# Kernel optimization log

Measured on AMD Instinct MI355X. Metric: run time of the kernel, lower is better.

The kernel has to match this reference:

```python
import jax, jax.numpy as jnp
import numpy as np
from jax import lax

B, T1, T2, C = 8, 128, 128, 256
K = 3

def setup_inputs() -> dict:
    key = jax.random.key(0)
    k1, k2, kw, kb = jax.random.split(key, 4)
    x1 = jax.random.normal(k1, (B, T1, C), dtype=jnp.float32)
    x2 = jax.random.normal(k2, (B, T2, C), dtype=jnp.float32)
    # conv2d: in_channels = 2C, out_channels = C, kernel 3x3 (OIHW)
    fan_in = 2 * C * K * K
    bound = 1.0 / np.sqrt(fan_in)
    W = jax.random.uniform(kw, (C, 2 * C, K, K), jnp.float32, -bound, bound)
    b = jax.random.uniform(kb, (C,), jnp.float32, -bound, bound)
    alpha = jnp.float32(0.5)
    return {"x1": x1, "x2": x2, "W": W, "b": b, "alpha": alpha}


def reference(x1, x2, W, b, alpha):
    # x1: [B, T1, C], x2: [B, T2, C]
    a = jnp.transpose(x1, (0, 2, 1))  # [B, C, T1]
    c2 = jnp.transpose(x2, (0, 2, 1))  # [B, C, T2]
    Bd, Cd, T1d = a.shape
    T2d = c2.shape[-1]
    # joint outer-product tensor: [B, 2C, T1, T2]
    j1 = jnp.broadcast_to(a[:, :, :, None], (Bd, Cd, T1d, T2d))
    j2 = jnp.broadcast_to(c2[:, :, None, :], (Bd, Cd, T1d, T2d))
    joint = jnp.concatenate([j1, j2], axis=1)
    out = lax.conv_general_dilated(
        joint, W, window_strides=(1, 1), padding="SAME",
        dimension_numbers=("NCHW", "OIHW", "NCHW"))
    out = out + b[None, :, None, None]
    out = jax.nn.gelu(out, approximate=False)  # torch nn.GELU default = exact erf
    out_T1 = jnp.mean(out, axis=-1)            # [B, C, T1]
    out_T1 = jnp.transpose(out_T1, (0, 2, 1))  # [B, T1, C]
    return out_T1 * alpha + x1
```

## Files before the change

### kernel.cpp

```cpp
#include <hip/hip_runtime.h>
#include <math.h>

#define B_   8
#define T_   128
#define C_   256
#define XLDP 136

typedef unsigned short ushort;
typedef ushort ushort8v __attribute__((ext_vector_type(8)));
typedef __bf16 bf16x8  __attribute__((ext_vector_type(8)));
typedef float  f32x4   __attribute__((ext_vector_type(4)));

__device__ __forceinline__ ushort f2bf(float f) {
    unsigned u = __float_as_uint(f);
    u += 0x7fffu + ((u >> 16) & 1u);
    return (ushort)(u >> 16);
}

__device__ __forceinline__ float gelu_fast(float x) {
    float x2 = x * x;
    float y2 = x * fmaf(-0.10294234f, x2, -2.30220818f);
    float e  = __builtin_amdgcn_exp2f(y2);
    return x * __builtin_amdgcn_rcpf(1.0f + e);
}

__global__ __launch_bounds__(256) void tc_pack(
    const float* __restrict__ x1, const float* __restrict__ x2,
    const float* __restrict__ W, ushort* __restrict__ Xp,
    ushort* __restrict__ Wt)
{
    const int bid = blockIdx.x, t = threadIdx.x;
    if (bid < 256) {
        __shared__ ushort lw[4608];
        const float* src = W + (size_t)bid * 4608;
        #pragma unroll
        for (int i = 0; i < 18; ++i)
            lw[t + i * 256] = f2bf(src[t + i * 256]);
        __syncthreads();
        #pragma unroll
        for (int i = 0; i < 18; ++i) {
            int d = t + i * 256;
            int c = d & 255;
            int row18 = d >> 8;
            int s = (row18 >= 9) ? 1 : 0;
            int r = row18 - s * 9;
            int rsrc = (s == 0) ? r : (r % 3) * 3 + (r / 3);
            Wt[(((size_t)s * 64 + (bid >> 2)) * 48 + (bid & 3) * 9 + r) * 256 + c]
                = lw[(s * 256 + c) * 9 + rsrc];
        }
    } else {
        int g = (bid - 256) * 256 + t;
        int e = g * 8;
        int s  = e >> 18;
        int me = e & 262143;
        const float* src = (s ? x2 : x1) + me;
        float4 lo = *(const float4*)src;
        float4 hi = *(const float4*)(src + 4);
        ushort8v u;
        u[0] = f2bf(lo.x); u[1] = f2bf(lo.y); u[2] = f2bf(lo.z); u[3] = f2bf(lo.w);
        u[4] = f2bf(hi.x); u[5] = f2bf(hi.y); u[6] = f2bf(hi.z); u[7] = f2bf(hi.w);
        *(ushort8v*)&Xp[e] = u;
    }
}

__global__ __launch_bounds__(256, 4) void tc_gemm(
    const ushort* __restrict__ Xp, const ushort* __restrict__ Wt,
    float* __restrict__ Sg)
{
    __shared__ ushort Xs[64 * XLDP];
    __shared__ ushort Ws[48 * XLDP];

    const int og = blockIdx.x;
    const int mh = blockIdx.y;
    const int tid = threadIdx.x;
    const int l = tid & 63, w = tid >> 6;
    const int r16 = l & 15, kb = l >> 4;

    ushort8v xb[2][4], wb[2][3];
    f32x4 acc[2][3] = {};

    auto loadr = [&](int r, int buf) {
        int s = r >> 1, p = r & 1;
        const ushort* xsrc = Xp + ((size_t)s * 1024 + mh * 64) * 256 + p * 128;
        #pragma unroll
        for (int j = 0; j < 4; ++j) {
            int c = tid + j * 256;
            xb[buf][j] = *(const ushort8v*)(xsrc + (size_t)(c >> 4) * 256 + (c & 15) * 8);
        }
        const ushort* wsrc = Wt + ((size_t)s * 64 + og) * 48 * 256 + p * 128;
        #pragma unroll
        for (int j = 0; j < 3; ++j) {
            int c = tid + j * 256;
            wb[buf][j] = *(const ushort8v*)(wsrc + (size_t)(c >> 4) * 256 + (c & 15) * 8);
        }
    };

    loadr(0, 0);

    #pragma unroll
    for (int r = 0; r < 4; ++r) {
        const int cur = r & 1, s = r >> 1;
        __syncthreads();
        #pragma unroll
        for (int j = 0; j < 4; ++j) {
            int c = tid + j * 256;
            *(ushort8v*)&Xs[(c >> 4) * XLDP + (c & 15) * 8] = xb[cur][j];
        }
        #pragma unroll
        for (int j = 0; j < 3; ++j) {
            int c = tid + j * 256;
            *(ushort8v*)&Ws[(c >> 4) * XLDP + (c & 15) * 8] = wb[cur][j];
        }
        if (r < 3) loadr(r + 1, cur ^ 1);
        __syncthreads();
        #pragma unroll
        for (int ks = 0; ks < 4; ++ks) {
            bf16x8 af = __builtin_bit_cast(bf16x8,
                *(const ushort8v*)&Xs[(w * 16 + r16) * XLDP + ks * 32 + kb * 8]);
            #pragma unroll
            for (int nf = 0; nf < 3; ++nf) {
                bf16x8 bfr = __builtin_bit_cast(bf16x8,
                    *(const ushort8v*)&Ws[(nf * 16 + r16) * XLDP + ks * 32 + kb * 8]);
                acc[s][nf] = __builtin_amdgcn_mfma_f32_16x16x32_bf16(af, bfr, acc[s][nf], 0, 0, 0);
            }
        }
    }

    #pragma unroll
    for (int s = 0; s < 2; ++s)
        #pragma unroll
        for (int nf = 0; nf < 3; ++nf) {
            int n = nf * 16 + r16;
            if (n < 36)
                *(f32x4*)&Sg[((size_t)(s * 64 + og) * 36 + n) * 1024
                             + mh * 64 + w * 16 + kb * 4] = acc[s][nf];
        }
}

__global__ __launch_bounds__(128) void tc_fin(
    const float* __restrict__ Sg, const float* __restrict__ x1,
    const float* __restrict__ bias, const float* __restrict__ alpha_p,
    float* __restrict__ out)
{
    const int o = blockIdx.x & 255;
    const int b = blockIdx.x >> 8;
    const int t = threadIdx.x;
    const int og = o >> 2, oo = o & 3;

    __shared__ float Bv[3][T_];

    const float* S0 = Sg + ((size_t)og * 36 + oo * 9) * 1024 + b * 128;
    const float* S1 = Sg + ((size_t)(64 + og) * 36 + oo * 9) * 1024 + b * 128;

    float a0 = 0.f, a1 = 0.f, a2 = 0.f;
    float b0 = 0.f, b1 = 0.f, b2 = 0.f;
    #pragma unroll
    for (int sh = 0; sh < 3; ++sh) {
        int row = t + sh - 1;
        if (row >= 0 && row < T_) {
            const float* p0 = S0 + sh * 3 * 1024 + row;
            a0 += p0[0]; a1 += p0[1024]; a2 += p0[2048];
            const float* p1 = S1 + sh * 3 * 1024 + row;
            b0 += p1[0]; b1 += p1[1024]; b2 += p1[2048];
        }
    }
    const float bo = bias[o];
    float A3 = bo + a0 + a1 + a2;
    float Al = bo + a1 + a2;
    float Ar = bo + a0 + a1;
    Bv[0][t] = b0 + b1 + b2;
    Bv[1][t] = b1 + b2;
    Bv[2][t] = b0 + b1;
    __syncthreads();

    int cls = (t == 0) ? 1 : ((t == T_ - 1) ? 2 : 0);
    const float* Bs = Bv[cls];
    float s0 = 0.f, s1 = 0.f, s2 = 0.f, s3 = 0.f;
    for (int j = 0; j < T_; j += 4) {
        f32x4 v = *(const f32x4*)&Bs[j];
        s0 += gelu_fast(A3 + v[0]); s1 += gelu_fast(A3 + v[1]);
        s2 += gelu_fast(A3 + v[2]); s3 += gelu_fast(A3 + v[3]);
    }
    float sm = (s0 + s1) + (s2 + s3);
    float bl = Bs[0], br = Bs[T_ - 1];
    sm += gelu_fast(Al + bl) - gelu_fast(A3 + bl);
    sm += gelu_fast(Ar + br) - gelu_fast(A3 + br);

    const float kk2 = (*alpha_p) * (1.0f / (float)T_);
    size_t go = ((size_t)(b * T_ + t)) * C_ + o;
    out[go] = sm * kk2 + x1[go];
}

extern "C" void kernel_launch(void* const* d_in, const int* in_sizes, int n_in,
                              void* d_out, int out_size, void* d_ws, size_t ws_size,
                              hipStream_t stream) {
    const float* x1    = (const float*)d_in[0];
    const float* x2    = (const float*)d_in[1];
    const float* W     = (const float*)d_in[2];
    const float* bias  = (const float*)d_in[3];
    const float* alpha = (const float*)d_in[4];
    float* out = (float*)d_out;

    float*  Sg = (float*)d_ws;
    ushort* Xp = (ushort*)((char*)d_ws + (size_t)2 * 64 * 36 * 1024 * 4);
    ushort* Wt = Xp + (size_t)2 * 1024 * 256;

    tc_pack<<<512, 256, 0, stream>>>(x1, x2, W, Xp, Wt);
    tc_gemm<<<dim3(64, 16), 256, 0, stream>>>(Xp, Wt, Sg);
    tc_fin<<<B_ * C_, T_, 0, stream>>>(Sg, x1, bias, alpha, out);
}
```

Before: 94.81 us.

## Fold time-shift reduction into GEMM K dimension via halo-padded X tile

The GEMM is reorganized so the three time-shifted taps are summed inside the MFMA K loop. The kernel loads a 66-row X tile with zero-padded halo and indexes it with a shift offset, using K=768 instead of writing 36 separate partial products per output group. Weights are repacked accordingly, and the grid becomes 12x16x2 with 64x64 tiles and a 2x2 warp layout. The finisher now reads 3 precomputed values per side instead of gathering and summing 9 shifted values, which cuts intermediate traffic. The cost is a larger shared-memory footprint and lower occupancy (launch bounds 3).

```diff
diff --git a/kernel.cpp b/kernel.cpp
--- a/kernel.cpp
+++ b/kernel.cpp
@@ -4,7 +4,8 @@
 #define B_   8
 #define T_   128
 #define C_   256
-#define XLDP 136
+#define XLDS 264
+#define WLDP 136
 
 typedef unsigned short ushort;
 typedef ushort ushort8v __attribute__((ext_vector_type(8)));
@@ -39,14 +40,15 @@
         __syncthreads();
         #pragma unroll
         for (int i = 0; i < 18; ++i) {
-            int d = t + i * 256;
-            int c = d & 255;
-            int row18 = d >> 8;
-            int s = (row18 >= 9) ? 1 : 0;
-            int r = row18 - s * 9;
-            int rsrc = (s == 0) ? r : (r % 3) * 3 + (r / 3);
-            Wt[(((size_t)s * 64 + (bid >> 2)) * 48 + (bid & 3) * 9 + r) * 256 + c]
-                = lw[(s * 256 + c) * 9 + rsrc];
+            int d  = t + i * 256;
+            int s  = d / 2304;
+            int e  = d - s * 2304;
+            int nj = e / 768;
+            int k  = e - nj * 768;
+            int sh = k >> 8, ci = k & 255;
+            ushort v = (s == 0) ? lw[ci * 9 + sh * 3 + nj]
+                                : lw[(256 + ci) * 9 + nj * 3 + sh];
+            Wt[((size_t)s * 768 + bid * 3 + nj) * 768 + k] = v;
         }
     } else {
         int g = (bid - 256) * 256 + t;
@@ -63,107 +65,115 @@
     }
 }
 
-__global__ __launch_bounds__(256, 4) void tc_gemm(
+__global__ __launch_bounds__(256, 3) void tc_gemm(
     const ushort* __restrict__ Xp, const ushort* __restrict__ Wt,
-    float* __restrict__ Sg)
+    float* __restrict__ AB)
 {
-    __shared__ ushort Xs[64 * XLDP];
-    __shared__ ushort Ws[48 * XLDP];
-
-    const int og = blockIdx.x;
-    const int mh = blockIdx.y;
-    const int tid = threadIdx.x;
-    const int l = tid & 63, w = tid >> 6;
+    __shared__ ushort Xs[66 * XLDS];
+    __shared__ ushort Ws[64 * WLDP];
+
+    const int tn = blockIdx.x;
+    const int tm = blockIdx.y;
+    const int s  = blockIdx.z;
+    const int u  = threadIdx.x;
+    const int l  = u & 63, w = u >> 6;
+    const int wr = w >> 1, wc = w & 1;
     const int r16 = l & 15, kb = l >> 4;
 
-    ushort8v xb[2][4], wb[2][3];
-    f32x4 acc[2][3] = {};
-
-    auto loadr = [&](int r, int buf) {
-        int s = r >> 1, p = r & 1;
-        const ushort* xsrc = Xp + ((size_t)s * 1024 + mh * 64) * 256 + p * 128;
+    const int b_     = tm >> 1;
+    const int t_base = (tm & 1) * 64;
+    const ushort* Xb = Xp + ((size_t)s * 1024 + b_ * T_) * C_;
+    const ushort* Wb = Wt + ((size_t)s * 768 + tn * 64) * 768;
+
+    {
+        ushort8v zero = {};
+        #pragma unroll
+        for (int j = 0; j < 9; ++j) {
+            int c = u + j * 256;
+            if (j < 8 || c < 2112) {
+                int i  = c >> 5;
+                int kc = (c & 31) * 8;
+                int t  = t_base + i - 1;
+                ushort8v v = (t >= 0 && t < T_)
+                           ? *(const ushort8v*)(Xb + (size_t)t * C_ + kc) : zero;
+                *(ushort8v*)&Xs[i * XLDS + kc] = v;
+            }
+        }
+    }
+
+    ushort8v wbuf[4];
+    #pragma unroll
+    for (int j = 0; j < 4; ++j) {
+        int c = u + j * 256;
+        wbuf[j] = *(const ushort8v*)(Wb + (size_t)(c >> 4) * 768 + (c & 15) * 8);
+    }
+
+    f32x4 acc[2][2] = {};
+    #pragma unroll
+    for (int r = 0; r < 6; ++r) {
+        const int sh = r >> 1, p = r & 1;
+        __syncthreads();
         #pragma unroll
         for (int j = 0; j < 4; ++j) {
-            int c = tid + j * 256;
-            xb[buf][j] = *(const ushort8v*)(xsrc + (size_t)(c >> 4) * 256 + (c & 15) * 8);
-        }
-        const ushort* wsrc = Wt + ((size_t)s * 64 + og) * 48 * 256 + p * 128;
-        #pragma unroll
-        for (int j = 0; j < 3; ++j) {
-            int c = tid + j * 256;
-            wb[buf][j] = *(const ushort8v*)(wsrc + (size_t)(c >> 4) * 256 + (c & 15) * 8);
-        }
-    };
-
-    loadr(0, 0);
+            int c = u + j * 256;
+            *(ushort8v*)&Ws[(c >> 4) * WLDP + (c & 15) * 8] = wbuf[j];
+        }
+        if (r < 5) {
+            const int rn = r + 1;
+            const ushort* wsrc = Wb + (rn >> 1) * 256 + (rn & 1) * 128;
+            #pragma unroll
+            for (int j = 0; j < 4; ++j) {
+                int c = u + j * 256;
+                wbuf[j] = *(const ushort8v*)(wsrc + (size_t)(c >> 4) * 768 + (c & 15) * 8);
+            }
+        }
+        __syncthreads();
+        #pragma unroll
+        for (int ks = 0; ks < 4; ++ks) {
+            const int ka = p * 128 + ks * 32 + kb * 8;
+            const int kw_ = ks * 32 + kb * 8;
+            bf16x8 a0 = __builtin_bit_cast(bf16x8,
+                *(const ushort8v*)&Xs[(wr * 32 + r16 + sh) * XLDS + ka]);
+            bf16x8 a1 = __builtin_bit_cast(bf16x8,
+                *(const ushort8v*)&Xs[(wr * 32 + 16 + r16 + sh) * XLDS + ka]);
+            bf16x8 b0 = __builtin_bit_cast(bf16x8,
+                *(const ushort8v*)&Ws[(wc * 32 + r16) * WLDP + kw_]);
+            bf16x8 b1 = __builtin_bit_cast(bf16x8,
+                *(const ushort8v*)&Ws[(wc * 32 + 16 + r16) * WLDP + kw_]);
+            acc[0][0] = __builtin_amdgcn_mfma_f32_16x16x32_bf16(a0, b0, acc[0][0], 0, 0, 0);
+            acc[0][1] = __builtin_amdgcn_mfma_f32_16x16x32_bf16(a0, b1, acc[0][1], 0, 0, 0);
+            acc[1][0] = __builtin_amdgcn_mfma_f32_16x16x32_bf16(a1, b0, acc[1][0], 0, 0, 0);
+            acc[1][1] = __builtin_amdgcn_mfma_f32_16x16x32_bf16(a1, b1, acc[1][1], 0, 0, 0);
+        }
+    }
 
     #pragma unroll
-    for (int r = 0; r < 4; ++r) {
-        const int cur = r & 1, s = r >> 1;
-        __syncthreads();
-        #pragma unroll
-        for (int j = 0; j < 4; ++j) {
-            int c = tid + j * 256;
-            *(ushort8v*)&Xs[(c >> 4) * XLDP + (c & 15) * 8] = xb[cur][j];
-        }
-        #pragma unroll
-        for (int j = 0; j < 3; ++j) {
-            int c = tid + j * 256;
-            *(ushort8v*)&Ws[(c >> 4) * XLDP + (c & 15) * 8] = wb[cur][j];
-        }
-        if (r < 3) loadr(r + 1, cur ^ 1);
-        __syncthreads();
-        #pragma unroll
-        for (int ks = 0; ks < 4; ++ks) {
-            bf16x8 af = __builtin_bit_cast(bf16x8,
-                *(const ushort8v*)&Xs[(w * 16 + r16) * XLDP + ks * 32 + kb * 8]);
-            #pragma unroll
-            for (int nf = 0; nf < 3; ++nf) {
-                bf16x8 bfr = __builtin_bit_cast(bf16x8,
-                    *(const ushort8v*)&Ws[(nf * 16 + r16) * XLDP + ks * 32 + kb * 8]);
-                acc[s][nf] = __builtin_amdgcn_mfma_f32_16x16x32_bf16(af, bfr, acc[s][nf], 0, 0, 0);
-            }
-        }
-    }
-
-    #pragma unroll
-    for (int s = 0; s < 2; ++s)
-        #pragma unroll
-        for (int nf = 0; nf < 3; ++nf) {
-            int n = nf * 16 + r16;
-            if (n < 36)
-                *(f32x4*)&Sg[((size_t)(s * 64 + og) * 36 + n) * 1024
-                             + mh * 64 + w * 16 + kb * 4] = acc[s][nf];
-        }
+    for (int j = 0; j < 2; ++j) {
+        int n = tn * 64 + wc * 32 + j * 16 + r16;
+        #pragma unroll
+        for (int i = 0; i < 2; ++i) {
+            int m = tm * 64 + wr * 32 + i * 16 + kb * 4;
+            *(f32x4*)&AB[((size_t)s * 768 + n) * 1024 + m] = acc[i][j];
+        }
+    }
 }
 
 __global__ __launch_bounds__(128) void tc_fin(
-    const float* __restrict__ Sg, const float* __restrict__ x1,
+    const float* __restrict__ AB, const float* __restrict__ x1,
     const float* __restrict__ bias, const float* __restrict__ alpha_p,
     float* __restrict__ out)
 {
     const int o = blockIdx.x & 255;
     const int b = blockIdx.x >> 8;
     const int t = threadIdx.x;
-    const int og = o >> 2, oo = o & 3;
 
     __shared__ float Bv[3][T_];
 
-    const float* S0 = Sg + ((size_t)og * 36 + oo * 9) * 1024 + b * 128;
-    const float* S1 = Sg + ((size_t)(64 + og) * 36 + oo * 9) * 1024 + b * 128;
-
-    float a0 = 0.f, a1 = 0.f, a2 = 0.f;
-    float b0 = 0.f, b1 = 0.f, b2 = 0.f;
-    #pragma unroll
-    for (int sh = 0; sh < 3; ++sh) {
-        int row = t + sh - 1;
-        if (row >= 0 && row < T_) {
-            const float* p0 = S0 + sh * 3 * 1024 + row;
-            a0 += p0[0]; a1 += p0[1024]; a2 += p0[2048];
-            const float* p1 = S1 + sh * 3 * 1024 + row;
-            b0 += p1[0]; b1 += p1[1024]; b2 += p1[2048];
-        }
-    }
+    const float* A0 = AB + ((size_t)o * 3) * 1024 + b * T_ + t;
+    const float* A1 = AB + ((size_t)768 + o * 3) * 1024 + b * T_ + t;
+    float a0 = A0[0], a1 = A0[1024], a2 = A0[2048];
+    float b0 = A1[0], b1 = A1[1024], b2 = A1[2048];
+
     const float bo = bias[o];
     float A3 = bo + a0 + a1 + a2;
     float Al = bo + a1 + a2;
@@ -201,11 +211,11 @@
     const float* alpha = (const float*)d_in[4];
     float* out = (float*)d_out;
 
-    float*  Sg = (float*)d_ws;
-    ushort* Xp = (ushort*)((char*)d_ws + (size_t)2 * 64 * 36 * 1024 * 4);
+    float*  AB = (float*)d_ws;
+    ushort* Xp = (ushort*)((char*)d_ws + (size_t)2 * 768 * 1024 * 4);
     ushort* Wt = Xp + (size_t)2 * 1024 * 256;
 
     tc_pack<<<512, 256, 0, stream>>>(x1, x2, W, Xp, Wt);
-    tc_gemm<<<dim3(64, 16), 256, 0, stream>>>(Xp, Wt, Sg);
-    tc_fin<<<B_ * C_, T_, 0, stream>>>(Sg, x1, bias, alpha, out);
-}
+    tc_gemm<<<dim3(12, 16, 2), 256, 0, stream>>>(Xp, Wt, AB);
+    tc_fin<<<B_ * C_, T_, 0, stream>>>(AB, x1, bias, alpha, out);
+}
```

After: 90.55 us. 4.5% less time.
